# Optimization experiments

Hardware: AMD Instinct MI355X
Metric: run time of the kernel (lower is better)

Reference implementation:

```python
import jax, jax.numpy as jnp
import numpy as np

N_NODES = 50000
D = 128
E_RAND = 640000
ALPHA = 0.2  # LeakyReLU negative slope


def setup_inputs() -> dict:
    key = jax.random.key(0)
    k1, k2, k3, k4, k5 = jax.random.split(key, 5)
    inputs = jax.random.normal(k1, (N_NODES, D), dtype=jnp.float32) * 0.1
    # xavier_normal with gain=1.414 as in the torch module
    W = jax.random.normal(k2, (D, D), dtype=jnp.float32) * (1.414 * np.sqrt(2.0 / (D + D)))
    a = jax.random.normal(k3, (2 * D,), dtype=jnp.float32) * (1.414 * np.sqrt(2.0 / (1 + 2 * D)))
    # random edges + self-loops so every node has at least one outgoing edge (nonzero rowsum)
    src = jnp.concatenate([jax.random.randint(k4, (E_RAND,), 0, N_NODES), jnp.arange(N_NODES)])
    dst = jnp.concatenate([jax.random.randint(k5, (E_RAND,), 0, N_NODES), jnp.arange(N_NODES)])
    edge = jnp.stack([src, dst]).astype(jnp.int64)
    return {"inputs": inputs, "edge": edge, "W": W, "a": a}


def reference(inputs, edge, W, a):
    N = inputs.shape[0]
    src, dst = edge[0], edge[1]
    h = inputs @ W  # [N, D]
    # a @ [h_src; h_dst] per edge == h_src @ a[:D] + h_dst @ a[D:]
    score = h[src] @ a[:D] + h[dst] @ a[D:]  # [E]
    edge_e = jnp.exp(jax.nn.leaky_relu(score, negative_slope=ALPHA))  # [E]
    # sparse.mm(coo(edge, edge_e), ones): rowsum over src (coalesce sums duplicates)
    e_rowsum = jax.ops.segment_sum(edge_e, src, num_segments=N)  # [N]
    # sparse.mm(coo(edge, edge_e), h): weighted aggregation of h[dst] into src rows
    h_prime = jax.ops.segment_sum(edge_e[:, None] * h[dst], src, num_segments=N)  # [N, D]
    h_prime = h_prime / e_rowsum[:, None]
    return jax.nn.elu(h_prime)
```

## Files before the change

kernel.cpp:

```cpp
#include <hip/hip_runtime.h>
#include <hip/hip_bf16.h>


constexpr int D  = 128;
constexpr int CH = 4096;

typedef __attribute__((ext_vector_type(8))) short bf16x8;
typedef __attribute__((ext_vector_type(4))) float f32x4;

__device__ __forceinline__ short f2bf(float f) {
    unsigned u = __float_as_uint(f);
    unsigned r = (u + 0x7fffu + ((u >> 16) & 1u)) >> 16;
    return (short)r;
}
__device__ __forceinline__ float bf2f(short b) {
    return __uint_as_float(((unsigned)(unsigned short)b) << 16);
}

__global__ __launch_bounds__(256) void prep_w(const float* __restrict__ W,
                                              short* __restrict__ bw) {
    const int tid = blockIdx.x * 256 + threadIdx.x;
    if (tid >= 2048) return;
    const int l = tid & 63, st = tid >> 6;
    const int s = st >> 3, t = st & 7;
    const int n = t * 16 + (l & 15);
    const int q = l >> 4;
#pragma unroll
    for (int j = 0; j < 8; ++j) {
        const int k = s * 32 + q * 8 + j;
        bw[tid * 8 + j] = f2bf(W[k * D + n]);
    }
}

__global__ __launch_bounds__(256) void gemm_mfma(const float* __restrict__ X,
                                                 const short* __restrict__ bw,
                                                 const float* __restrict__ a,
                                                 short* __restrict__ h,
                                                 float* __restrict__ s1,
                                                 float* __restrict__ s2, int N) {
    const int wave = threadIdx.x >> 6, lane = threadIdx.x & 63;
    const int r0 = blockIdx.x * 64 + wave * 16;
    const int m = lane & 15, q = lane >> 4;
    const int arow = r0 + m;
    const bool rowok = arow < N;
    const float* xp = X + (size_t)arow * D + q * 8;

    f32x4 acc[8] = {};
#pragma unroll
    for (int s = 0; s < 4; ++s) {
        float4 xa = {0, 0, 0, 0}, xb = {0, 0, 0, 0};
        if (rowok) {
            xa = *(const float4*)(xp + s * 32);
            xb = *(const float4*)(xp + s * 32 + 4);
        }
        bf16x8 af;
        af[0] = f2bf(xa.x); af[1] = f2bf(xa.y); af[2] = f2bf(xa.z); af[3] = f2bf(xa.w);
        af[4] = f2bf(xb.x); af[5] = f2bf(xb.y); af[6] = f2bf(xb.z); af[7] = f2bf(xb.w);
#pragma unroll
        for (int t = 0; t < 8; ++t) {
            bf16x8 bf = *(const bf16x8*)(bw + ((s * 8 + t) * 64 + lane) * 8);
            acc[t] = __builtin_amdgcn_mfma_f32_16x16x32_bf16(af, bf, acc[t], 0, 0, 0);
        }
    }
    float a1v[8], a2v[8];
#pragma unroll
    for (int t = 0; t < 8; ++t) {
        a1v[t] = a[t * 16 + m];
        a2v[t] = a[D + t * 16 + m];
    }
    float p1[4] = {0, 0, 0, 0}, p2[4] = {0, 0, 0, 0};
#pragma unroll
    for (int t = 0; t < 8; ++t) {
#pragma unroll
        for (int i = 0; i < 4; ++i) {
            const int row = r0 + q * 4 + i;
            const short hb = f2bf(acc[t][i]);
            if (row < N) h[(size_t)row * D + t * 16 + m] = hb;
            const float hr = bf2f(hb);
            p1[i] += hr * a1v[t];
            p2[i] += hr * a2v[t];
        }
    }
#pragma unroll
    for (int off = 1; off < 16; off <<= 1) {
#pragma unroll
        for (int i = 0; i < 4; ++i) {
            p1[i] += __shfl_xor(p1[i], off);
            p2[i] += __shfl_xor(p2[i], off);
        }
    }
    if (m < 4) {
        const int row = r0 + q * 4 + m;
        if (row < N) {
            const float v1 = (m == 0) ? p1[0] : (m == 1) ? p1[1] : (m == 2) ? p1[2] : p1[3];
            const float v2 = (m == 0) ? p2[0] : (m == 1) ? p2[1] : (m == 2) ? p2[2] : p2[3];
            s1[row] = v1;
            s2[row] = v2;
        }
    }
}

__global__ __launch_bounds__(256) void bin_count(const int* __restrict__ src,
                                                 int* __restrict__ cell_cnt,
                                                 int NBK, int NC, int E) {
    __shared__ int hist[256];
    const int c = blockIdx.x, t = threadIdx.x;
    hist[t] = 0;
    __syncthreads();
    const int lo = c * CH, hi = min(lo + CH, E);
    const int hi4 = lo + ((hi - lo) & ~3);
    for (int i = lo + t * 4; i < hi4; i += 1024) {
        const int4 s4 = *(const int4*)(src + i);
        atomicAdd(&hist[s4.x >> 8], 1);
        atomicAdd(&hist[s4.y >> 8], 1);
        atomicAdd(&hist[s4.z >> 8], 1);
        atomicAdd(&hist[s4.w >> 8], 1);
    }
    for (int i = hi4 + t; i < hi; i += 256)
        atomicAdd(&hist[src[i] >> 8], 1);
    __syncthreads();
    for (int b = t; b < NBK; b += 256)
        cell_cnt[b * NC + c] = hist[b];
}

__global__ __launch_bounds__(256) void scan_block(const int* __restrict__ counts,
                                                  int* __restrict__ offsets,
                                                  int* __restrict__ blocksums, int N) {
    __shared__ int lsum[256];
    const int b = blockIdx.x, t = threadIdx.x;
    const int i0 = b * 1024 + t * 4;
    int c[4];
#pragma unroll
    for (int j = 0; j < 4; ++j) c[j] = (i0 + j < N) ? counts[i0 + j] : 0;
    lsum[t] = c[0] + c[1] + c[2] + c[3];
    __syncthreads();
    for (int off = 1; off < 256; off <<= 1) {
        int v = (t >= off) ? lsum[t - off] : 0;
        __syncthreads();
        lsum[t] += v;
        __syncthreads();
    }
    int run = (t == 0) ? 0 : lsum[t - 1];
#pragma unroll
    for (int j = 0; j < 4; ++j) {
        if (i0 + j < N) offsets[i0 + j] = run;
        run += c[j];
    }
    if (t == 255) blocksums[b] = lsum[255];
}

__global__ __launch_bounds__(256) void scan_top(const int* __restrict__ blocksums,
                                                int* __restrict__ blockpref, int G) {
    __shared__ int lsum[256];
    const int t = threadIdx.x;
    int v = (t < G) ? blocksums[t] : 0;
    lsum[t] = v;
    __syncthreads();
    for (int off = 1; off < 256; off <<= 1) {
        int u = (t >= off) ? lsum[t - off] : 0;
        __syncthreads();
        lsum[t] += u;
        __syncthreads();
    }
    if (t < G) blockpref[t] = lsum[t] - v;
}

__device__ __forceinline__ int cellbase(const int* __restrict__ co,
                                        const int* __restrict__ cp, int cell) {
    return co[cell] + cp[cell >> 10];
}

__global__ __launch_bounds__(256) void bin_scatter(
    const int* __restrict__ src, const int* __restrict__ dst,
    const int* __restrict__ cell_off, const int* __restrict__ cell_pref,
    int2* __restrict__ binned, int NBK, int NC, int E) {
    __shared__ int cnt[256];
    const int c = blockIdx.x, t = threadIdx.x;
    cnt[t] = 0;
    __syncthreads();
    const int lo = c * CH, hi = min(lo + CH, E);
    const int hi4 = lo + ((hi - lo) & ~3);
    for (int i = lo + t * 4; i < hi4; i += 1024) {
        const int4 s4 = *(const int4*)(src + i);
        const int4 d4 = *(const int4*)(dst + i);
        const int sv[4] = {s4.x, s4.y, s4.z, s4.w};
        const int dv[4] = {d4.x, d4.y, d4.z, d4.w};
#pragma unroll
        for (int j = 0; j < 4; ++j) {
            const int b = sv[j] >> 8;
            const int r = atomicAdd(&cnt[b], 1);
            binned[cellbase(cell_off, cell_pref, b * NC + c) + r] = make_int2(sv[j], dv[j]);
        }
    }
    for (int i = hi4 + t; i < hi; i += 256) {
        const int s = src[i];
        const int b = s >> 8;
        const int r = atomicAdd(&cnt[b], 1);
        binned[cellbase(cell_off, cell_pref, b * NC + c) + r] = make_int2(s, dst[i]);
    }
}

__global__ __launch_bounds__(256) void fine_scatter(
    const int2* __restrict__ binned,
    const int* __restrict__ cell_off, const int* __restrict__ cell_pref,
    int* __restrict__ offsets, int* __restrict__ csrd,
    int NBK, int NC, int N, int E) {
    __shared__ int ncnt[256], snc[256], exclp[256], pcnt[256];
    const int b = blockIdx.x, t = threadIdx.x;
    const int start = cellbase(cell_off, cell_pref, b * NC);
    const int end = (b + 1 < NBK) ? cellbase(cell_off, cell_pref, (b + 1) * NC) : E;
    ncnt[t] = 0;
    pcnt[t] = 0;
    __syncthreads();
    for (int i = start + t; i < end; i += 256)
        atomicAdd(&ncnt[binned[i].x & 255], 1);
    __syncthreads();
    snc[t] = ncnt[t];
    __syncthreads();
    for (int off = 1; off < 256; off <<= 1) {
        int v = (t >= off) ? snc[t - off] : 0;
        __syncthreads();
        snc[t] += v;
        __syncthreads();
    }
    exclp[t] = snc[t] - ncnt[t];
    const int node = b * 256 + t;
    if (node < N) offsets[node] = start + exclp[t];
    if (b == NBK - 1 && t == 0) offsets[N] = E;
    __syncthreads();
    for (int i = start + t; i < end; i += 256) {
        const int2 e = binned[i];
        const int r = e.x & 255;
        csrd[start + exclp[r] + atomicAdd(&pcnt[r], 1)] = e.y;
    }
}

__global__ __launch_bounds__(256) void aggregate(
    const int* __restrict__ csrd, const int* __restrict__ offsets,
    const float* __restrict__ s1, const float* __restrict__ s2,
    const short* __restrict__ h, float* __restrict__ out, int N) {
    const int n    = blockIdx.x * 4 + (threadIdx.x >> 6);
    const int lane = threadIdx.x & 63;
    if (n >= N) return;
    const int g = lane >> 4, m = lane & 15;
    const int beg = offsets[n];
    const int end = offsets[n + 1];
    const float s1n = s1[n];

    int   d0  = csrd[min(beg + g, end - 1)];
    int   d1  = csrd[min(beg + 4 + g, end - 1)];
    float s20 = s2[d0];

    float acc[8] = {};
    float rs = 0.f;
    for (int k0 = beg; k0 < end; k0 += 4) {
        const int   d2  = csrd[min(k0 + 8 + g, end - 1)];
        const float s21 = s2[d1];
        const bf16x8 row = *(const bf16x8*)(h + (size_t)d0 * D + m * 8);
        float sc = s1n + s20;
        sc = sc > 0.f ? sc : 0.2f * sc;
        float ee = __expf(sc);
        if (k0 + g >= end) ee = 0.f;
#pragma unroll
        for (int j = 0; j < 8; ++j)
            acc[j] += ee * bf2f(row[j]);
        rs += ee;
        d0 = d1; d1 = d2; s20 = s21;
    }
#pragma unroll
    for (int off = 16; off <= 32; off <<= 1) {
        rs += __shfl_xor(rs, off);
#pragma unroll
        for (int j = 0; j < 8; ++j) acc[j] += __shfl_xor(acc[j], off);
    }
    if (g == 0) {
        const float inv = 1.f / rs;
        float o[8];
#pragma unroll
        for (int j = 0; j < 8; ++j) {
            float v = acc[j] * inv;
            o[j] = v > 0.f ? v : expm1f(v);
        }
        float* op = out + (size_t)n * D + m * 8;
        *(float4*)op       = make_float4(o[0], o[1], o[2], o[3]);
        *(float4*)(op + 4) = make_float4(o[4], o[5], o[6], o[7]);
    }
}

extern "C" void kernel_launch(void* const* d_in, const int* in_sizes, int n_in,
                              void* d_out, int out_size, void* d_ws, size_t ws_size,
                              hipStream_t stream) {
    const float* X    = (const float*)d_in[0];
    const int*   edge = (const int*)d_in[1];
    const float* W    = (const float*)d_in[2];
    const float* a    = (const float*)d_in[3];
    float* out = (float*)d_out;

    const int N = in_sizes[0] / D;
    const int E = in_sizes[1] / 2;
    const int* src = edge;
    const int* dst = edge + E;

    const int NBK = (N + 255) >> 8;
    const int NC  = (E + CH - 1) / CH;
    const int cells = NBK * NC;
    const int GsC = (cells + 1023) / 1024;

    char* ws = (char*)d_ws;
    short* h     = (short*)ws; ws += (size_t)N * D * sizeof(short);
    int2* binned = (int2*)ws;  ws += (size_t)E * sizeof(int2);
    int* csrd    = (int*)ws;   ws += (size_t)E * sizeof(int);
    short* bw    = (short*)ws; ws += 2048 * 8 * sizeof(short);
    float* s1    = (float*)ws; ws += (size_t)N * sizeof(float);
    float* s2    = (float*)ws; ws += (size_t)N * sizeof(float);
    int* offsets = (int*)ws;   ws += (size_t)(N + 1) * sizeof(int);
    int* cell_cnt = (int*)ws;  ws += (size_t)cells * sizeof(int);
    int* cell_off = (int*)ws;  ws += (size_t)cells * sizeof(int);
    int* bsumsC  = (int*)ws;   ws += 256 * sizeof(int);
    int* bprefC  = (int*)ws;   ws += 256 * sizeof(int);

    prep_w<<<8, 256, 0, stream>>>(W, bw);
    gemm_mfma<<<(N + 63) / 64, 256, 0, stream>>>(X, bw, a, h, s1, s2, N);
    bin_count<<<NC, 256, 0, stream>>>(src, cell_cnt, NBK, NC, E);
    scan_block<<<GsC, 256, 0, stream>>>(cell_cnt, cell_off, bsumsC, cells);
    scan_top<<<1, 256, 0, stream>>>(bsumsC, bprefC, GsC);
    bin_scatter<<<NC, 256, 0, stream>>>(src, dst, cell_off, bprefC, binned, NBK, NC, E);
    fine_scatter<<<NBK, 256, 0, stream>>>(binned, cell_off, bprefC, offsets, csrd, NBK, NC, N, E);
    aggregate<<<(N + 3) / 4, 256, 0, stream>>>(csrd, offsets, s1, s2, h, out, N);
}
```

Baseline: 158.1 us.

## Merge prep/count and gemm/bin-scatter kernels, fold top scan, prefetch rows

Merges the W-prep kernel into the bin-count launch and the GEMM into the bin-scatter launch as extra blocks. The single-block top scan is removed; each scatter block recomputes the block prefixes with a wave shuffle scan. Together this cuts the launch count from eight to five and lets independent work share one grid. It also switches to packed bf16 conversion and prefetches the next h row in the aggregate loop, which costs extra registers and some redundant scan work per block.

```diff
diff --git a/kernel.cpp b/kernel.cpp
--- a/kernel.cpp
+++ b/kernel.cpp
@@ -16,94 +16,31 @@
 __device__ __forceinline__ float bf2f(short b) {
     return __uint_as_float(((unsigned)(unsigned short)b) << 16);
 }
-
-__global__ __launch_bounds__(256) void prep_w(const float* __restrict__ W,
-                                              short* __restrict__ bw) {
-    const int tid = blockIdx.x * 256 + threadIdx.x;
-    if (tid >= 2048) return;
-    const int l = tid & 63, st = tid >> 6;
-    const int s = st >> 3, t = st & 7;
-    const int n = t * 16 + (l & 15);
-    const int q = l >> 4;
-#pragma unroll
-    for (int j = 0; j < 8; ++j) {
-        const int k = s * 32 + q * 8 + j;
-        bw[tid * 8 + j] = f2bf(W[k * D + n]);
-    }
-}
-
-__global__ __launch_bounds__(256) void gemm_mfma(const float* __restrict__ X,
-                                                 const short* __restrict__ bw,
-                                                 const float* __restrict__ a,
-                                                 short* __restrict__ h,
-                                                 float* __restrict__ s1,
-                                                 float* __restrict__ s2, int N) {
-    const int wave = threadIdx.x >> 6, lane = threadIdx.x & 63;
-    const int r0 = blockIdx.x * 64 + wave * 16;
-    const int m = lane & 15, q = lane >> 4;
-    const int arow = r0 + m;
-    const bool rowok = arow < N;
-    const float* xp = X + (size_t)arow * D + q * 8;
-
-    f32x4 acc[8] = {};
-#pragma unroll
-    for (int s = 0; s < 4; ++s) {
-        float4 xa = {0, 0, 0, 0}, xb = {0, 0, 0, 0};
-        if (rowok) {
-            xa = *(const float4*)(xp + s * 32);
-            xb = *(const float4*)(xp + s * 32 + 4);
-        }
-        bf16x8 af;
-        af[0] = f2bf(xa.x); af[1] = f2bf(xa.y); af[2] = f2bf(xa.z); af[3] = f2bf(xa.w);
-        af[4] = f2bf(xb.x); af[5] = f2bf(xb.y); af[6] = f2bf(xb.z); af[7] = f2bf(xb.w);
-#pragma unroll
-        for (int t = 0; t < 8; ++t) {
-            bf16x8 bf = *(const bf16x8*)(bw + ((s * 8 + t) * 64 + lane) * 8);
-            acc[t] = __builtin_amdgcn_mfma_f32_16x16x32_bf16(af, bf, acc[t], 0, 0, 0);
-        }
-    }
-    float a1v[8], a2v[8];
-#pragma unroll
-    for (int t = 0; t < 8; ++t) {
-        a1v[t] = a[t * 16 + m];
-        a2v[t] = a[D + t * 16 + m];
-    }
-    float p1[4] = {0, 0, 0, 0}, p2[4] = {0, 0, 0, 0};
-#pragma unroll
-    for (int t = 0; t < 8; ++t) {
-#pragma unroll
-        for (int i = 0; i < 4; ++i) {
-            const int row = r0 + q * 4 + i;
-            const short hb = f2bf(acc[t][i]);
-            if (row < N) h[(size_t)row * D + t * 16 + m] = hb;
-            const float hr = bf2f(hb);
-            p1[i] += hr * a1v[t];
-            p2[i] += hr * a2v[t];
-        }
-    }
-#pragma unroll
-    for (int off = 1; off < 16; off <<= 1) {
-#pragma unroll
-        for (int i = 0; i < 4; ++i) {
-            p1[i] += __shfl_xor(p1[i], off);
-            p2[i] += __shfl_xor(p2[i], off);
-        }
-    }
-    if (m < 4) {
-        const int row = r0 + q * 4 + m;
-        if (row < N) {
-            const float v1 = (m == 0) ? p1[0] : (m == 1) ? p1[1] : (m == 2) ? p1[2] : p1[3];
-            const float v2 = (m == 0) ? p2[0] : (m == 1) ? p2[1] : (m == 2) ? p2[2] : p2[3];
-            s1[row] = v1;
-            s2[row] = v2;
-        }
-    }
-}
-
-__global__ __launch_bounds__(256) void bin_count(const int* __restrict__ src,
-                                                 int* __restrict__ cell_cnt,
-                                                 int NBK, int NC, int E) {
+__device__ __forceinline__ short2 pk_bf16(float x, float y) {
+    __hip_bfloat162 bb = __float22bfloat162_rn(make_float2(x, y));
+    short2 r;
+    __builtin_memcpy(&r, &bb, 4);
+    return r;
+}
+
+__global__ __launch_bounds__(256) void prep_and_count(
+    const float* __restrict__ W, short* __restrict__ bw,
+    const int* __restrict__ src, int* __restrict__ cell_cnt,
+    int NBK, int NC, int E) {
     __shared__ int hist[256];
+    if (blockIdx.x >= NC) {
+        const int tid = (blockIdx.x - NC) * 256 + threadIdx.x;
+        const int l = tid & 63, st = tid >> 6;
+        const int s = st >> 3, t = st & 7;
+        const int n = t * 16 + (l & 15);
+        const int q = l >> 4;
+#pragma unroll
+        for (int j = 0; j < 8; ++j) {
+            const int k = s * 32 + q * 8 + j;
+            bw[tid * 8 + j] = f2bf(W[k * D + n]);
+        }
+        return;
+    }
     const int c = blockIdx.x, t = threadIdx.x;
     hist[t] = 0;
     __syncthreads();
@@ -149,69 +86,141 @@
     if (t == 255) blocksums[b] = lsum[255];
 }
 
-__global__ __launch_bounds__(256) void scan_top(const int* __restrict__ blocksums,
-                                                int* __restrict__ blockpref, int G) {
-    __shared__ int lsum[256];
+__device__ __forceinline__ void top_scan(const int* __restrict__ bsums, int GsC,
+                                         int* bpref) {
     const int t = threadIdx.x;
-    int v = (t < G) ? blocksums[t] : 0;
-    lsum[t] = v;
-    __syncthreads();
-    for (int off = 1; off < 256; off <<= 1) {
-        int u = (t >= off) ? lsum[t - off] : 0;
-        __syncthreads();
-        lsum[t] += u;
-        __syncthreads();
-    }
-    if (t < G) blockpref[t] = lsum[t] - v;
-}
-
-__device__ __forceinline__ int cellbase(const int* __restrict__ co,
-                                        const int* __restrict__ cp, int cell) {
-    return co[cell] + cp[cell >> 10];
-}
-
-__global__ __launch_bounds__(256) void bin_scatter(
+    if (t < 64) {
+        int v = (t < GsC) ? bsums[t] : 0;
+        int inc = v;
+#pragma unroll
+        for (int off = 1; off < 64; off <<= 1) {
+            int u = __shfl_up(inc, off);
+            if (t >= off) inc += u;
+        }
+        bpref[t] = inc - v;
+    }
+}
+
+__global__ __launch_bounds__(256) void gemm_and_binscatter(
+    const float* __restrict__ X, const short* __restrict__ bw,
+    const float* __restrict__ a, short* __restrict__ h,
+    float* __restrict__ s1, float* __restrict__ s2,
     const int* __restrict__ src, const int* __restrict__ dst,
-    const int* __restrict__ cell_off, const int* __restrict__ cell_pref,
-    int2* __restrict__ binned, int NBK, int NC, int E) {
+    const int* __restrict__ cell_off, const int* __restrict__ bsums,
+    int2* __restrict__ binned, int NBK, int NC, int GsC, int N, int E) {
     __shared__ int cnt[256];
-    const int c = blockIdx.x, t = threadIdx.x;
-    cnt[t] = 0;
-    __syncthreads();
-    const int lo = c * CH, hi = min(lo + CH, E);
-    const int hi4 = lo + ((hi - lo) & ~3);
-    for (int i = lo + t * 4; i < hi4; i += 1024) {
-        const int4 s4 = *(const int4*)(src + i);
-        const int4 d4 = *(const int4*)(dst + i);
-        const int sv[4] = {s4.x, s4.y, s4.z, s4.w};
-        const int dv[4] = {d4.x, d4.y, d4.z, d4.w};
-#pragma unroll
-        for (int j = 0; j < 4; ++j) {
-            const int b = sv[j] >> 8;
+    __shared__ int bpref[64];
+    if (blockIdx.x < (unsigned)NC) {
+        const int c = blockIdx.x, t = threadIdx.x;
+        cnt[t] = 0;
+        top_scan(bsums, GsC, bpref);
+        __syncthreads();
+        const int lo = c * CH, hi = min(lo + CH, E);
+        const int hi4 = lo + ((hi - lo) & ~3);
+        for (int i = lo + t * 4; i < hi4; i += 1024) {
+            const int4 s4 = *(const int4*)(src + i);
+            const int4 d4 = *(const int4*)(dst + i);
+            const int sv[4] = {s4.x, s4.y, s4.z, s4.w};
+            const int dv[4] = {d4.x, d4.y, d4.z, d4.w};
+#pragma unroll
+            for (int j = 0; j < 4; ++j) {
+                const int b = sv[j] >> 8;
+                const int cell = b * NC + c;
+                const int r = atomicAdd(&cnt[b], 1);
+                binned[cell_off[cell] + bpref[cell >> 10] + r] = make_int2(sv[j], dv[j]);
+            }
+        }
+        for (int i = hi4 + t; i < hi; i += 256) {
+            const int s = src[i];
+            const int b = s >> 8;
+            const int cell = b * NC + c;
             const int r = atomicAdd(&cnt[b], 1);
-            binned[cellbase(cell_off, cell_pref, b * NC + c) + r] = make_int2(sv[j], dv[j]);
-        }
-    }
-    for (int i = hi4 + t; i < hi; i += 256) {
-        const int s = src[i];
-        const int b = s >> 8;
-        const int r = atomicAdd(&cnt[b], 1);
-        binned[cellbase(cell_off, cell_pref, b * NC + c) + r] = make_int2(s, dst[i]);
+            binned[cell_off[cell] + bpref[cell >> 10] + r] = make_int2(s, dst[i]);
+        }
+        return;
+    }
+    const int wave = threadIdx.x >> 6, lane = threadIdx.x & 63;
+    const int r0 = (blockIdx.x - NC) * 64 + wave * 16;
+    const int m = lane & 15, q = lane >> 4;
+    const int arow = r0 + m;
+    const bool rowok = arow < N;
+    const float* xp = X + (size_t)arow * D + q * 8;
+
+    f32x4 acc[8] = {};
+#pragma unroll
+    for (int s = 0; s < 4; ++s) {
+        float4 xa = {0, 0, 0, 0}, xb = {0, 0, 0, 0};
+        if (rowok) {
+            xa = *(const float4*)(xp + s * 32);
+            xb = *(const float4*)(xp + s * 32 + 4);
+        }
+        bf16x8 af;
+        short2 c0 = pk_bf16(xa.x, xa.y), c1 = pk_bf16(xa.z, xa.w);
+        short2 c2 = pk_bf16(xb.x, xb.y), c3 = pk_bf16(xb.z, xb.w);
+        af[0] = c0.x; af[1] = c0.y; af[2] = c1.x; af[3] = c1.y;
+        af[4] = c2.x; af[5] = c2.y; af[6] = c3.x; af[7] = c3.y;
+#pragma unroll
+        for (int t = 0; t < 8; ++t) {
+            bf16x8 bf = *(const bf16x8*)(bw + ((s * 8 + t) * 64 + lane) * 8);
+            acc[t] = __builtin_amdgcn_mfma_f32_16x16x32_bf16(af, bf, acc[t], 0, 0, 0);
+        }
+    }
+    float a1v[8], a2v[8];
+#pragma unroll
+    for (int t = 0; t < 8; ++t) {
+        a1v[t] = a[t * 16 + m];
+        a2v[t] = a[D + t * 16 + m];
+    }
+    float p1[4] = {0, 0, 0, 0}, p2[4] = {0, 0, 0, 0};
+#pragma unroll
+    for (int t = 0; t < 8; ++t) {
+        short2 h01 = pk_bf16(acc[t][0], acc[t][1]);
+        short2 h23 = pk_bf16(acc[t][2], acc[t][3]);
+        const short hb[4] = {h01.x, h01.y, h23.x, h23.y};
+#pragma unroll
+        for (int i = 0; i < 4; ++i) {
+            const int row = r0 + q * 4 + i;
+            if (row < N) h[(size_t)row * D + t * 16 + m] = hb[i];
+            const float hr = bf2f(hb[i]);
+            p1[i] += hr * a1v[t];
+            p2[i] += hr * a2v[t];
+        }
+    }
+#pragma unroll
+    for (int off = 1; off < 16; off <<= 1) {
+#pragma unroll
+        for (int i = 0; i < 4; ++i) {
+            p1[i] += __shfl_xor(p1[i], off);
+            p2[i] += __shfl_xor(p2[i], off);
+        }
+    }
+    if (m < 4) {
+        const int row = r0 + q * 4 + m;
+        if (row < N) {
+            const float v1 = (m == 0) ? p1[0] : (m == 1) ? p1[1] : (m == 2) ? p1[2] : p1[3];
+            const float v2 = (m == 0) ? p2[0] : (m == 1) ? p2[1] : (m == 2) ? p2[2] : p2[3];
+            s1[row] = v1;
+            s2[row] = v2;
+        }
     }
 }
 
 __global__ __launch_bounds__(256) void fine_scatter(
     const int2* __restrict__ binned,
-    const int* __restrict__ cell_off, const int* __restrict__ cell_pref,
+    const int* __restrict__ cell_off, const int* __restrict__ bsums,
     int* __restrict__ offsets, int* __restrict__ csrd,
-    int NBK, int NC, int N, int E) {
+    int NBK, int NC, int GsC, int N, int E) {
     __shared__ int ncnt[256], snc[256], exclp[256], pcnt[256];
+    __shared__ int bpref[64];
     const int b = blockIdx.x, t = threadIdx.x;
-    const int start = cellbase(cell_off, cell_pref, b * NC);
-    const int end = (b + 1 < NBK) ? cellbase(cell_off, cell_pref, (b + 1) * NC) : E;
     ncnt[t] = 0;
     pcnt[t] = 0;
-    __syncthreads();
+    top_scan(bsums, GsC, bpref);
+    __syncthreads();
+    const int cell0 = b * NC;
+    const int start = cell_off[cell0] + bpref[cell0 >> 10];
+    const int cell1 = (b + 1) * NC;
+    const int end = (b + 1 < NBK) ? cell_off[cell1] + bpref[cell1 >> 10] : E;
     for (int i = start + t; i < end; i += 256)
         atomicAdd(&ncnt[binned[i].x & 255], 1);
     __syncthreads();
@@ -250,22 +259,23 @@
     int   d0  = csrd[min(beg + g, end - 1)];
     int   d1  = csrd[min(beg + 4 + g, end - 1)];
     float s20 = s2[d0];
+    bf16x8 row0 = *(const bf16x8*)(h + (size_t)d0 * D + m * 8);
 
     float acc[8] = {};
     float rs = 0.f;
     for (int k0 = beg; k0 < end; k0 += 4) {
-        const int   d2  = csrd[min(k0 + 8 + g, end - 1)];
-        const float s21 = s2[d1];
-        const bf16x8 row = *(const bf16x8*)(h + (size_t)d0 * D + m * 8);
+        const int    d2   = csrd[min(k0 + 8 + g, end - 1)];
+        const float  s21  = s2[d1];
+        const bf16x8 row1 = *(const bf16x8*)(h + (size_t)d1 * D + m * 8);
         float sc = s1n + s20;
         sc = sc > 0.f ? sc : 0.2f * sc;
         float ee = __expf(sc);
         if (k0 + g >= end) ee = 0.f;
 #pragma unroll
         for (int j = 0; j < 8; ++j)
-            acc[j] += ee * bf2f(row[j]);
+            acc[j] += ee * bf2f(row0[j]);
         rs += ee;
-        d0 = d1; d1 = d2; s20 = s21;
+        d0 = d1; d1 = d2; s20 = s21; row0 = row1;
     }
 #pragma unroll
     for (int off = 16; off <= 32; off <<= 1) {
@@ -305,26 +315,26 @@
     const int NC  = (E + CH - 1) / CH;
     const int cells = NBK * NC;
     const int GsC = (cells + 1023) / 1024;
+    const int NG  = (N + 63) / 64;
 
     char* ws = (char*)d_ws;
-    short* h     = (short*)ws; ws += (size_t)N * D * sizeof(short);
-    int2* binned = (int2*)ws;  ws += (size_t)E * sizeof(int2);
-    int* csrd    = (int*)ws;   ws += (size_t)E * sizeof(int);
-    short* bw    = (short*)ws; ws += 2048 * 8 * sizeof(short);
-    float* s1    = (float*)ws; ws += (size_t)N * sizeof(float);
-    float* s2    = (float*)ws; ws += (size_t)N * sizeof(float);
-    int* offsets = (int*)ws;   ws += (size_t)(N + 1) * sizeof(int);
-    int* cell_cnt = (int*)ws;  ws += (size_t)cells * sizeof(int);
-    int* cell_off = (int*)ws;  ws += (size_t)cells * sizeof(int);
-    int* bsumsC  = (int*)ws;   ws += 256 * sizeof(int);
-    int* bprefC  = (int*)ws;   ws += 256 * sizeof(int);
-
-    prep_w<<<8, 256, 0, stream>>>(W, bw);
-    gemm_mfma<<<(N + 63) / 64, 256, 0, stream>>>(X, bw, a, h, s1, s2, N);
-    bin_count<<<NC, 256, 0, stream>>>(src, cell_cnt, NBK, NC, E);
+    short* h      = (short*)ws; ws += (size_t)N * D * sizeof(short);
+    int2* binned  = (int2*)ws;  ws += (size_t)E * sizeof(int2);
+    int* csrd     = (int*)ws;   ws += (size_t)E * sizeof(int);
+    short* bw     = (short*)ws; ws += 2048 * 8 * sizeof(short);
+    float* s1     = (float*)ws; ws += (size_t)N * sizeof(float);
+    float* s2     = (float*)ws; ws += (size_t)N * sizeof(float);
+    int* offsets  = (int*)ws;   ws += (size_t)(N + 1) * sizeof(int);
+    int* cell_cnt = (int*)ws;   ws += (size_t)cells * sizeof(int);
+    int* cell_off = (int*)ws;   ws += (size_t)cells * sizeof(int);
+    int* bsumsC   = (int*)ws;   ws += 256 * sizeof(int);
+
+    prep_and_count<<<NC + 8, 256, 0, stream>>>(W, bw, src, cell_cnt, NBK, NC, E);
     scan_block<<<GsC, 256, 0, stream>>>(cell_cnt, cell_off, bsumsC, cells);
-    scan_top<<<1, 256, 0, stream>>>(bsumsC, bprefC, GsC);
-    bin_scatter<<<NC, 256, 0, stream>>>(src, dst, cell_off, bprefC, binned, NBK, NC, E);
-    fine_scatter<<<NBK, 256, 0, stream>>>(binned, cell_off, bprefC, offsets, csrd, NBK, NC, N, E);
+    gemm_and_binscatter<<<NC + NG, 256, 0, stream>>>(X, bw, a, h, s1, s2, src, dst,
+                                                     cell_off, bsumsC, binned,
+                                                     NBK, NC, GsC, N, E);
+    fine_scatter<<<NBK, 256, 0, stream>>>(binned, cell_off, bsumsC, offsets, csrd,
+                                          NBK, NC, GsC, N, E);
     aggregate<<<(N + 3) / 4, 256, 0, stream>>>(csrd, offsets, s1, s2, h, out, N);
 }
```

New measurement: 147.8 us. 6.6% less time.
